# Optimization experiments

Measured on AMD Instinct MI355X. Metric: run time of the kernel, lower is better.

Reference implementation:

```python
import jax, jax.numpy as jnp
import numpy as np

K_GRID = 20          # grid side -> n1 = 400 nodes, n2 = 760 edges
CONTEXT = 512
HIDDEN = 2 * CONTEXT # per module: hidden_dim = 2*context_size
BATCH = 4096
RHO = 1.0            # ADMM penalty
N_ITERS = 50         # fixed ADMM iterations (differentiable unroll)


def _grid_incidence(k):
    """Node-arc incidence of a k x k grid DAG (right + down edges)."""
    n = k * k
    edges = []
    for i in range(k):
        for j in range(k):
            u = i * k + j
            if j + 1 < k:
                edges.append((u, i * k + j + 1))
            if i + 1 < k:
                edges.append((u, (i + 1) * k + j))
    m = len(edges)
    A = np.zeros((n, m), np.float32)
    for e, (u, v) in enumerate(edges):
        A[u, e] = 1.0   # outflow
        A[v, e] = -1.0  # inflow
    b = np.zeros(n, np.float32)
    b[0] = 1.0      # source
    b[n - 1] = -1.0 # sink
    return A, b


def setup_inputs() -> dict:
    key = jax.random.key(0)
    k_d, k_w1, k_b1, k_w2, k_b2 = jax.random.split(key, 5)
    A_np, b_np = _grid_incidence(K_GRID)
    n2 = A_np.shape[1]
    d = jax.random.normal(k_d, (BATCH, CONTEXT), dtype=jnp.float32)
    s1 = 1.0 / np.sqrt(CONTEXT)
    s2 = 1.0 / np.sqrt(HIDDEN)
    W1 = jax.random.uniform(k_w1, (HIDDEN, CONTEXT), jnp.float32, -s1, s1)
    b1 = jax.random.uniform(k_b1, (HIDDEN,), jnp.float32, -s1, s1)
    W2 = jax.random.uniform(k_w2, (n2, HIDDEN), jnp.float32, -s2, s2)
    b2 = jax.random.uniform(k_b2, (n2,), jnp.float32, -s2, s2)
    return {"d": d, "W1": W1, "b1": b1, "W2": W2, "b2": b2,
            "A": jnp.asarray(A_np), "b_eq": jnp.asarray(b_np)}


def reference(d, W1, b1, W2, b2, A, b_eq):
    # MLP router: fc_1 -> LeakyReLU(0.1) -> fc_2
    h = d @ W1.T + b1
    h = jnp.where(h >= 0, h, 0.1 * h)
    w = h @ W2.T + b2  # [B, n2] edge costs

    # QP: min_x w^T x + 0.5||x||^2  s.t.  A x = b_eq, x >= 0
    # Batched ADMM with equality-constrained x-update (KKT solve via pinv(AA^T)).
    M = jnp.linalg.pinv(A @ A.T)  # [n1, n1], symmetric
    z = jnp.zeros_like(w)
    u = jnp.zeros_like(w)
    x = jnp.zeros_like(w)

    def step(carry, _):
        x, z, u = carry
        v = RHO * (z - u) - w                       # [B, n2]
        nu = (v @ A.T - (1.0 + RHO) * b_eq) @ M     # [B, n1] dual of Ax=b
        x = (v - nu @ A) / (1.0 + RHO)              # satisfies A x = b
        z = jnp.maximum(x + u, 0.0)                 # projection onto x >= 0
        u = u + x - z
        return (x, z, u), None

    (x, z, u), _ = jax.lax.scan(step, (x, z, u), None, length=N_ITERS)
    return x  # [B, n2], primal solution (matches CvxpyLayer's variable x)
```

## Files before the change

kernel.cpp:

```cpp
#include <hip/hip_runtime.h>

#define KG 20
#define N1 400
#define N2 760
#define BATCH 4096
#define NITER 50
#define PI_F 3.14159265897932f

typedef __attribute__((ext_vector_type(8))) short bf16x8;
typedef __attribute__((ext_vector_type(4))) float f32x4;

#define WSYNC() asm volatile("s_waitcnt lgkmcnt(0)" ::: "memory")

__device__ __forceinline__ float bf2f(unsigned short u) {
    unsigned int x = ((unsigned int)u) << 16;
    union { unsigned int i; float f; } c; c.i = x; return c.f;
}
__device__ __forceinline__ unsigned short f2bf(float f) {
    union { float f; unsigned int i; } c; c.f = f;
    unsigned int r = c.i + 0x7FFFu + ((c.i >> 16) & 1u);
    return (unsigned short)(r >> 16);
}

constexpr double CPI = 3.14159265358979323846;
constexpr double ccos(double x) {
    constexpr double TP = 6.28318530717958647692;
    long long k = (long long)(x / TP);
    double r = x - (double)k * TP;
    if (r > CPI)  r -= TP;
    if (r < -CPI) r += TP;
    double r2 = r * r, term = 1.0, s = 1.0;
    for (int n = 1; n <= 15; ++n) { term *= -r2 / ((2.0 * n - 1.0) * (2.0 * n)); s += term; }
    return s;
}
struct Tbl { float phi[20][20]; float lam[20]; };
constexpr Tbl mk_tbl() {
    Tbl t{};
    for (int i = 0; i < 20; ++i)
        for (int a = 0; a < 20; ++a) {
            double na = (a == 0) ? 0.22360679774997896964 : 0.31622776601683793320;
            t.phi[i][a] = (float)(na * ccos(CPI * (double)a * ((double)i + 0.5) / 20.0));
        }
    for (int a = 0; a < 20; ++a) t.lam[a] = (float)(2.0 - 2.0 * ccos(CPI * (double)a / 20.0));
    return t;
}
static constexpr Tbl TB = mk_tbl();

__global__ void detect_dtype(const float* beq_as_f32, int* flag) {
    if (threadIdx.x == 0) {
        float v = beq_as_f32[0];
        *flag = (v > 0.5f && v < 1.5f) ? 0 : 1;
    }
}

__global__ void conv_biases(const void* b1, const void* b2, float* b1f, float* b2f,
                            const int* flag) {
    int i = blockIdx.x * 256 + threadIdx.x;
    int f = *flag;
    if (i < 1024)
        b1f[i] = f ? bf2f(((const unsigned short*)b1)[i]) : ((const float*)b1)[i];
    else if (i < 1024 + 760) {
        int j = i - 1024;
        b2f[j] = f ? bf2f(((const unsigned short*)b2)[j]) : ((const float*)b2)[j];
    }
}

template<bool LEAKY>
__global__ __launch_bounds__(256) void gemm_bt_bf16(
        const void* __restrict__ A,
        const void* __restrict__ B,
        const float* __restrict__ bias,
        unsigned short* __restrict__ C,
        int M, int N, int K, const int* __restrict__ flagp, int aUseFlag) {
    __shared__ unsigned short As[128 * 34];
    __shared__ unsigned short Bs[64 * 34];
    const int f   = *flagp;
    const int aBf = aUseFlag ? f : 1;
    const int bBf = f;
    const int tid  = threadIdx.x;
    const int m0   = blockIdx.x * 128;
    const int n0   = blockIdx.y * 64;
    const int wave = tid >> 6, lane = tid & 63;
    const int wm   = (wave & 1) * 64, wn = (wave >> 1) * 32;
    const int fr   = lane & 15;
    const int kc   = (lane >> 4) * 8;

    const int ra = tid >> 1, ca = (tid & 1) * 16;
    const int rb = tid >> 2, cb = (tid & 3) * 8;
    const int rbg = (n0 + rb < N) ? (n0 + rb) : (N - 1);

    f32x4 acc[4][2];
#pragma unroll
    for (int a = 0; a < 4; a++)
#pragma unroll
        for (int b = 0; b < 2; b++) acc[a][b] = (f32x4){0.f, 0.f, 0.f, 0.f};

    for (int k0 = 0; k0 < K; k0 += 32) {
        size_t aoff = (size_t)(m0 + ra) * K + k0 + ca;
        uint4 av0, av1;
        if (aBf) {
            av0 = *(const uint4*)&((const unsigned short*)A)[aoff];
            av1 = *(const uint4*)&((const unsigned short*)A)[aoff + 8];
        } else {
            const float* Af = (const float*)A;
            float4 f0 = *(const float4*)&Af[aoff];
            float4 f1 = *(const float4*)&Af[aoff + 4];
            float4 f2 = *(const float4*)&Af[aoff + 8];
            float4 f3 = *(const float4*)&Af[aoff + 12];
            av0.x = ((unsigned)f2bf(f0.y) << 16) | f2bf(f0.x);
            av0.y = ((unsigned)f2bf(f0.w) << 16) | f2bf(f0.z);
            av0.z = ((unsigned)f2bf(f1.y) << 16) | f2bf(f1.x);
            av0.w = ((unsigned)f2bf(f1.w) << 16) | f2bf(f1.z);
            av1.x = ((unsigned)f2bf(f2.y) << 16) | f2bf(f2.x);
            av1.y = ((unsigned)f2bf(f2.w) << 16) | f2bf(f2.z);
            av1.z = ((unsigned)f2bf(f3.y) << 16) | f2bf(f3.x);
            av1.w = ((unsigned)f2bf(f3.w) << 16) | f2bf(f3.z);
        }
        size_t boff = (size_t)rbg * K + k0 + cb;
        uint4 bv;
        if (bBf) bv = *(const uint4*)&((const unsigned short*)B)[boff];
        else {
            const float* Bf = (const float*)B;
            float4 f0 = *(const float4*)&Bf[boff];
            float4 f1 = *(const float4*)&Bf[boff + 4];
            bv.x = ((unsigned)f2bf(f0.y) << 16) | f2bf(f0.x);
            bv.y = ((unsigned)f2bf(f0.w) << 16) | f2bf(f0.z);
            bv.z = ((unsigned)f2bf(f1.y) << 16) | f2bf(f1.x);
            bv.w = ((unsigned)f2bf(f1.w) << 16) | f2bf(f1.z);
        }
        *(uint4*)&As[ra * 34 + ca]     = av0;
        *(uint4*)&As[ra * 34 + ca + 8] = av1;
        *(uint4*)&Bs[rb * 34 + cb]     = bv;
        __syncthreads();

        bf16x8 af[4], bfm[2];
#pragma unroll
        for (int a = 0; a < 4; a++) af[a]  = *(const bf16x8*)&As[(wm + a * 16 + fr) * 34 + kc];
#pragma unroll
        for (int b = 0; b < 2; b++) bfm[b] = *(const bf16x8*)&Bs[(wn + b * 16 + fr) * 34 + kc];
#pragma unroll
        for (int a = 0; a < 4; a++)
#pragma unroll
            for (int b = 0; b < 2; b++)
                acc[a][b] = __builtin_amdgcn_mfma_f32_16x16x32_bf16(af[a], bfm[b], acc[a][b], 0, 0, 0);
        __syncthreads();
    }
#pragma unroll
    for (int a = 0; a < 4; a++)
#pragma unroll
        for (int b = 0; b < 2; b++) {
            int col = n0 + wn + b * 16 + (lane & 15);
            if (col < N) {
                float bs = bias[col];
#pragma unroll
                for (int r = 0; r < 4; r++) {
                    int row = m0 + wm + a * 16 + (lane >> 4) * 4 + r;
                    float v = acc[a][b][r] + bs;
                    if (LEAKY) v = v >= 0.f ? v : 0.1f * v;
                    C[(size_t)row * N + col] = f2bf(v);
                }
            }
        }
}

#define SREG 448
__global__ __launch_bounds__(256, 2) void admm_kernel(
        const unsigned short* __restrict__ wglob,
        void* __restrict__ out, const int* __restrict__ flagp) {
    __shared__ float buf[8 * SREG];

    const int tid  = threadIdx.x;
    const int wid  = tid >> 6;
    const int lane = tid & 63;
    const int q    = lane >> 5;
    const int li   = lane & 31;
    const int sample = blockIdx.x * 8 + wid * 2 + q;
    const int flag = *flagp;

    if (li < 20) {
        const int i = li;
        float* B = &buf[(wid * 2 + q) * SREG];
        const size_t gb = (size_t)sample * N2;

        float wh[20], wv[20];
        if (i < 19) {
#pragma unroll
            for (int j = 0; j < 19; ++j) {
                wh[j] = bf2f(wglob[gb + 39 * i + 2 * j]);
                wv[j] = bf2f(wglob[gb + 39 * i + 2 * j + 1]);
            }
            wh[19] = 0.f;
            wv[19] = bf2f(wglob[gb + 39 * i + 38]);
        } else {
#pragma unroll
            for (int j = 0; j < 19; ++j) { wh[j] = bf2f(wglob[gb + 741 + j]); wv[j] = 0.f; }
            wh[19] = 0.f; wv[19] = 0.f;
        }

        float g[20];
        {
            float lamB = 2.f - 2.f * cosf(PI_F * (float)li / 20.f);
#pragma unroll
            for (int a = 0; a < 20; ++a) g[a] = 1.f / (TB.lam[a] + lamB);
            if (li == 0) g[0] = 0.f;
        }

        float sh[20], sv[20];
#pragma unroll
        for (int j = 0; j < 20; ++j) { sh[j] = 0.f; sv[j] = 0.f; }

        const int rup = (i > 0)  ? i - 1 : 0;
        const int rdn = (i < 19) ? i + 1 : i;

#pragma unroll 1
        for (int it = 0; it < NITER; ++it) {
            float vh[20], vv[20];
#pragma unroll
            for (int j = 0; j < 20; ++j) {
                vh[j] = fabsf(sh[j]) - wh[j];
                vv[j] = fabsf(sv[j]) - wv[j];
            }
#pragma unroll
            for (int j = 0; j < 20; j += 4)
                *(f32x4*)&B[20 * i + j] = (f32x4){vv[j], vv[j + 1], vv[j + 2], vv[j + 3]};
            WSYNC();
            float vvUp[20];
#pragma unroll
            for (int j = 0; j < 20; j += 4) {
                f32x4 t = *(f32x4*)&B[20 * rup + j];
                vvUp[j] = t[0]; vvUp[j + 1] = t[1]; vvUp[j + 2] = t[2]; vvUp[j + 3] = t[3];
            }
            WSYNC();
            float r[20];
#pragma unroll
            for (int j = 0; j < 20; ++j) {
                float acc = ((j < 19) ? vh[j] : 0.f) + vv[j];
                if (j > 0) acc -= vh[j - 1];
                acc -= (i > 0) ? vvUp[j] : 0.f;
                r[j] = acc;
            }
            r[0]  -= (i == 0)  ? 2.f : 0.f;
            r[19] += (i == 19) ? 2.f : 0.f;

            float e[10], o[10];
#pragma unroll
            for (int jj = 0; jj < 10; ++jj) { e[jj] = r[jj] + r[19 - jj]; o[jj] = r[jj] - r[19 - jj]; }
#pragma unroll
            for (int b = 0; b < 20; ++b) {
                float a;
                if ((b & 1) == 0) {
                    a = e[0] * TB.phi[0][b];
#pragma unroll
                    for (int jj = 1; jj < 10; ++jj) a += e[jj] * TB.phi[jj][b];
                } else {
                    a = o[0] * TB.phi[0][b];
#pragma unroll
                    for (int jj = 1; jj < 10; ++jj) a += o[jj] * TB.phi[jj][b];
                }
                B[22 * b + i] = a;
            }
            WSYNC();
            float t2[20];
#pragma unroll
            for (int k = 0; k < 20; k += 2) {
                float2 p = *(const float2*)&B[22 * li + k];
                t2[k] = p.x; t2[k + 1] = p.y;
            }
            WSYNC();
            float e2[10], o2[10];
#pragma unroll
            for (int kk = 0; kk < 10; ++kk) { e2[kk] = t2[kk] + t2[19 - kk]; o2[kk] = t2[kk] - t2[19 - kk]; }
            float v2[20];
#pragma unroll
            for (int a = 0; a < 20; ++a) {
                float acc;
                if ((a & 1) == 0) {
                    acc = e2[0] * TB.phi[0][a];
#pragma unroll
                    for (int kk = 1; kk < 10; ++kk) acc += e2[kk] * TB.phi[kk][a];
                } else {
                    acc = o2[0] * TB.phi[0][a];
#pragma unroll
                    for (int kk = 1; kk < 10; ++kk) acc += o2[kk] * TB.phi[kk][a];
                }
                v2[a] = acc * g[a];
            }
#pragma unroll
            for (int ii = 0; ii < 10; ++ii) {
                float E = v2[0] * TB.phi[ii][0];
#pragma unroll
                for (int m = 1; m < 10; ++m) E += v2[2 * m] * TB.phi[ii][2 * m];
                float O = v2[1] * TB.phi[ii][1];
#pragma unroll
                for (int m = 1; m < 10; ++m) O += v2[2 * m + 1] * TB.phi[ii][2 * m + 1];
                B[22 * ii + i]        = E + O;
                B[22 * (19 - ii) + i] = E - O;
            }
            WSYNC();
            float t3[20];
#pragma unroll
            for (int b = 0; b < 20; b += 2) {
                float2 p = *(const float2*)&B[22 * li + b];
                t3[b] = p.x; t3[b + 1] = p.y;
            }
            WSYNC();
            float nu[20];
#pragma unroll
            for (int jj = 0; jj < 10; ++jj) {
                float E = t3[0] * TB.phi[jj][0];
#pragma unroll
                for (int m = 1; m < 10; ++m) E += t3[2 * m] * TB.phi[jj][2 * m];
                float O = t3[1] * TB.phi[jj][1];
#pragma unroll
                for (int m = 1; m < 10; ++m) O += t3[2 * m + 1] * TB.phi[jj][2 * m + 1];
                nu[jj]      = E + O;
                nu[19 - jj] = E - O;
            }
#pragma unroll
            for (int j = 0; j < 20; j += 4)
                *(f32x4*)&B[20 * i + j] = (f32x4){nu[j], nu[j + 1], nu[j + 2], nu[j + 3]};
            WSYNC();
            float nuDn[20];
#pragma unroll
            for (int j = 0; j < 20; j += 4) {
                f32x4 t = *(f32x4*)&B[20 * rdn + j];
                nuDn[j] = t[0]; nuDn[j + 1] = t[1]; nuDn[j + 2] = t[2]; nuDn[j + 3] = t[3];
            }
            WSYNC();
#pragma unroll
            for (int j = 0; j < 20; ++j) {
                float xv = 0.5f * (vv[j] - nu[j] + nuDn[j]);
                sv[j] = xv + fminf(sv[j], 0.f);
                float xh = 0.f;
                if (j < 19) {
                    xh = 0.5f * (vh[j] - nu[j] + nu[j + 1]);
                    sh[j] = xh + fminf(sh[j], 0.f);
                }
                if (it == NITER - 1) {
                    if (i < 19) {
                        if (j < 19) {
                            if (flag) {
                                ((unsigned short*)out)[gb + 39 * i + 2 * j]     = f2bf(xh);
                                ((unsigned short*)out)[gb + 39 * i + 2 * j + 1] = f2bf(xv);
                            } else {
                                ((float*)out)[gb + 39 * i + 2 * j]     = xh;
                                ((float*)out)[gb + 39 * i + 2 * j + 1] = xv;
                            }
                        } else {
                            if (flag) ((unsigned short*)out)[gb + 39 * i + 38] = f2bf(xv);
                            else      ((float*)out)[gb + 39 * i + 38] = xv;
                        }
                    } else if (j < 19) {
                        if (flag) ((unsigned short*)out)[gb + 741 + j] = f2bf(xh);
                        else      ((float*)out)[gb + 741 + j] = xh;
                    }
                }
            }
        }
    }
}

extern "C" void kernel_launch(void* const* d_in, const int* in_sizes, int n_in,
                              void* d_out, int out_size, void* d_ws, size_t ws_size,
                              hipStream_t stream) {
    (void)in_sizes; (void)n_in; (void)out_size; (void)ws_size;
    const void* d   = d_in[0];
    const void* W1  = d_in[1];
    const void* b1  = d_in[2];
    const void* W2  = d_in[3];
    const void* b2  = d_in[4];
    const void* beq = d_in[6];

    char* ws = (char*)d_ws;
    int*            flag  = (int*)ws;
    float*          b1_f  = (float*)(ws + 256);
    float*          b2_f  = (float*)(ws + 4608);
    unsigned short* h_bf  = (unsigned short*)(ws + 8192);
    unsigned short* w_bf  = (unsigned short*)(ws + 8396800);

    detect_dtype<<<1, 64, 0, stream>>>((const float*)beq, flag);
    conv_biases<<<7, 256, 0, stream>>>(b1, b2, b1_f, b2_f, flag);

    gemm_bt_bf16<true ><<<dim3(32, 16), 256, 0, stream>>>(d,    W1, b1_f, h_bf, 4096, 1024, 512,  flag, 1);
    gemm_bt_bf16<false><<<dim3(32, 12), 256, 0, stream>>>(h_bf, W2, b2_f, w_bf, 4096, 760,  1024, flag, 0);

    admm_kernel<<<BATCH / 8, 256, 0, stream>>>(w_bf, d_out, flag);
}
```

Before: 349.4 us.

## Inline dtype detection, register-prefetch GEMM tiles, and hand-code DCT MACs with immediates

Drops the separate dtype-detection and bias-conversion kernels: each kernel now reads b_eq directly to infer dtype and converts the bias inline, which removes two launches. The GEMM loads the next k-tile into registers before computing on the current tile in shared memory, overlapping global loads with MFMA work. The DCT transforms in the ADMM loop are rewritten as inline-asm v_mul/v_fmac chains with literal constant operands so table coefficients never occupy registers. The inline asm may block compiler scheduling, and the halved table relies on the even/odd symmetry of the basis.

```diff
diff --git a/kernel.cpp b/kernel.cpp
--- a/kernel.cpp
+++ b/kernel.cpp
@@ -5,7 +5,7 @@
 #define N2 760
 #define BATCH 4096
 #define NITER 50
-#define PI_F 3.14159265897932f
+#define PI_F 3.14159265358979f
 
 typedef __attribute__((ext_vector_type(8))) short bf16x8;
 typedef __attribute__((ext_vector_type(4))) float f32x4;
@@ -33,10 +33,10 @@
     for (int n = 1; n <= 15; ++n) { term *= -r2 / ((2.0 * n - 1.0) * (2.0 * n)); s += term; }
     return s;
 }
-struct Tbl { float phi[20][20]; float lam[20]; };
+struct Tbl { float phi[10][20]; float lam[20]; };
 constexpr Tbl mk_tbl() {
     Tbl t{};
-    for (int i = 0; i < 20; ++i)
+    for (int i = 0; i < 10; ++i)
         for (int a = 0; a < 20; ++a) {
             double na = (a == 0) ? 0.22360679774997896964 : 0.31622776601683793320;
             t.phi[i][a] = (float)(na * ccos(CPI * (double)a * ((double)i + 0.5) / 20.0));
@@ -46,35 +46,44 @@
 }
 static constexpr Tbl TB = mk_tbl();
 
-__global__ void detect_dtype(const float* beq_as_f32, int* flag) {
-    if (threadIdx.x == 0) {
-        float v = beq_as_f32[0];
-        *flag = (v > 0.5f && v < 1.5f) ? 0 : 1;
-    }
-}
-
-__global__ void conv_biases(const void* b1, const void* b2, float* b1f, float* b2f,
-                            const int* flag) {
-    int i = blockIdx.x * 256 + threadIdx.x;
-    int f = *flag;
-    if (i < 1024)
-        b1f[i] = f ? bf2f(((const unsigned short*)b1)[i]) : ((const float*)b1)[i];
-    else if (i < 1024 + 760) {
-        int j = i - 1024;
-        b2f[j] = f ? bf2f(((const unsigned short*)b2)[j]) : ((const float*)b2)[j];
-    }
+#define CBITS(c) ((int)__builtin_bit_cast(unsigned int, (float)(c)))
+#define VMUL(d, c, s) asm("v_mul_f32 %0, %1, %2"  : "=v"(d) : "i"(CBITS(c)), "v"(s))
+#define VMAC(d, c, s) asm("v_fmac_f32 %0, %1, %2" : "+v"(d) : "i"(CBITS(c)), "v"(s))
+
+#define MACC10(acc, a, B) do { \
+    VMUL(acc, TB.phi[0][B], a[0]); VMAC(acc, TB.phi[1][B], a[1]); \
+    VMAC(acc, TB.phi[2][B], a[2]); VMAC(acc, TB.phi[3][B], a[3]); \
+    VMAC(acc, TB.phi[4][B], a[4]); VMAC(acc, TB.phi[5][B], a[5]); \
+    VMAC(acc, TB.phi[6][B], a[6]); VMAC(acc, TB.phi[7][B], a[7]); \
+    VMAC(acc, TB.phi[8][B], a[8]); VMAC(acc, TB.phi[9][B], a[9]); } while (0)
+#define MACE10(acc, a, II) do { \
+    VMUL(acc, TB.phi[II][0],  a[0]);  VMAC(acc, TB.phi[II][2],  a[2]); \
+    VMAC(acc, TB.phi[II][4],  a[4]);  VMAC(acc, TB.phi[II][6],  a[6]); \
+    VMAC(acc, TB.phi[II][8],  a[8]);  VMAC(acc, TB.phi[II][10], a[10]); \
+    VMAC(acc, TB.phi[II][12], a[12]); VMAC(acc, TB.phi[II][14], a[14]); \
+    VMAC(acc, TB.phi[II][16], a[16]); VMAC(acc, TB.phi[II][18], a[18]); } while (0)
+#define MACO10(acc, a, II) do { \
+    VMUL(acc, TB.phi[II][1],  a[1]);  VMAC(acc, TB.phi[II][3],  a[3]); \
+    VMAC(acc, TB.phi[II][5],  a[5]);  VMAC(acc, TB.phi[II][7],  a[7]); \
+    VMAC(acc, TB.phi[II][9],  a[9]);  VMAC(acc, TB.phi[II][11], a[11]); \
+    VMAC(acc, TB.phi[II][13], a[13]); VMAC(acc, TB.phi[II][15], a[15]); \
+    VMAC(acc, TB.phi[II][17], a[17]); VMAC(acc, TB.phi[II][19], a[19]); } while (0)
+
+__device__ __forceinline__ int detect_flag(const float* beqf) {
+    float v = beqf[0];
+    return (v > 0.5f && v < 1.5f) ? 0 : 1;
 }
 
 template<bool LEAKY>
 __global__ __launch_bounds__(256) void gemm_bt_bf16(
         const void* __restrict__ A,
         const void* __restrict__ B,
-        const float* __restrict__ bias,
+        const void* __restrict__ biasRaw,
         unsigned short* __restrict__ C,
-        int M, int N, int K, const int* __restrict__ flagp, int aUseFlag) {
+        int M, int N, int K, const float* __restrict__ beqf, int aUseFlag) {
     __shared__ unsigned short As[128 * 34];
     __shared__ unsigned short Bs[64 * 34];
-    const int f   = *flagp;
+    const int f   = detect_flag(beqf);
     const int aBf = aUseFlag ? f : 1;
     const int bBf = f;
     const int tid  = threadIdx.x;
@@ -89,15 +98,9 @@
     const int rb = tid >> 2, cb = (tid & 3) * 8;
     const int rbg = (n0 + rb < N) ? (n0 + rb) : (N - 1);
 
-    f32x4 acc[4][2];
-#pragma unroll
-    for (int a = 0; a < 4; a++)
-#pragma unroll
-        for (int b = 0; b < 2; b++) acc[a][b] = (f32x4){0.f, 0.f, 0.f, 0.f};
-
-    for (int k0 = 0; k0 < K; k0 += 32) {
+    uint4 av0, av1, bv;
+    auto load_tiles = [&](int k0) {
         size_t aoff = (size_t)(m0 + ra) * K + k0 + ca;
-        uint4 av0, av1;
         if (aBf) {
             av0 = *(const uint4*)&((const unsigned short*)A)[aoff];
             av1 = *(const uint4*)&((const unsigned short*)A)[aoff + 8];
@@ -117,7 +120,6 @@
             av1.w = ((unsigned)f2bf(f3.w) << 16) | f2bf(f3.z);
         }
         size_t boff = (size_t)rbg * K + k0 + cb;
-        uint4 bv;
         if (bBf) bv = *(const uint4*)&((const unsigned short*)B)[boff];
         else {
             const float* Bf = (const float*)B;
@@ -128,11 +130,24 @@
             bv.z = ((unsigned)f2bf(f1.y) << 16) | f2bf(f1.x);
             bv.w = ((unsigned)f2bf(f1.w) << 16) | f2bf(f1.z);
         }
+    };
+
+    f32x4 acc[4][2];
+#pragma unroll
+    for (int a = 0; a < 4; a++)
+#pragma unroll
+        for (int b = 0; b < 2; b++) acc[a][b] = (f32x4){0.f, 0.f, 0.f, 0.f};
+
+    load_tiles(0);
+    for (int k0 = 0; k0 < K; k0 += 32) {
         *(uint4*)&As[ra * 34 + ca]     = av0;
         *(uint4*)&As[ra * 34 + ca + 8] = av1;
         *(uint4*)&Bs[rb * 34 + cb]     = bv;
         __syncthreads();
 
+        int kn = (k0 + 32 < K) ? (k0 + 32) : k0;
+        load_tiles(kn);
+
         bf16x8 af[4], bfm[2];
 #pragma unroll
         for (int a = 0; a < 4; a++) af[a]  = *(const bf16x8*)&As[(wm + a * 16 + fr) * 34 + kc];
@@ -151,7 +166,8 @@
         for (int b = 0; b < 2; b++) {
             int col = n0 + wn + b * 16 + (lane & 15);
             if (col < N) {
-                float bs = bias[col];
+                float bs = f ? bf2f(((const unsigned short*)biasRaw)[col])
+                             : ((const float*)biasRaw)[col];
 #pragma unroll
                 for (int r = 0; r < 4; r++) {
                     int row = m0 + wm + a * 16 + (lane >> 4) * 4 + r;
@@ -166,7 +182,7 @@
 #define SREG 448
 __global__ __launch_bounds__(256, 2) void admm_kernel(
         const unsigned short* __restrict__ wglob,
-        void* __restrict__ out, const int* __restrict__ flagp) {
+        void* __restrict__ out, const float* __restrict__ beqf) {
     __shared__ float buf[8 * SREG];
 
     const int tid  = threadIdx.x;
@@ -175,7 +191,7 @@
     const int q    = lane >> 5;
     const int li   = lane & 31;
     const int sample = blockIdx.x * 8 + wid * 2 + q;
-    const int flag = *flagp;
+    const int flag = detect_flag(beqf);
 
     if (li < 20) {
         const int i = li;
@@ -245,20 +261,19 @@
             float e[10], o[10];
 #pragma unroll
             for (int jj = 0; jj < 10; ++jj) { e[jj] = r[jj] + r[19 - jj]; o[jj] = r[jj] - r[19 - jj]; }
-#pragma unroll
-            for (int b = 0; b < 20; ++b) {
-                float a;
-                if ((b & 1) == 0) {
-                    a = e[0] * TB.phi[0][b];
-#pragma unroll
-                    for (int jj = 1; jj < 10; ++jj) a += e[jj] * TB.phi[jj][b];
-                } else {
-                    a = o[0] * TB.phi[0][b];
-#pragma unroll
-                    for (int jj = 1; jj < 10; ++jj) a += o[jj] * TB.phi[jj][b];
-                }
-                B[22 * b + i] = a;
-            }
+            float t1[20];
+            MACC10(t1[0],  e, 0);  MACC10(t1[1],  o, 1);
+            MACC10(t1[2],  e, 2);  MACC10(t1[3],  o, 3);
+            MACC10(t1[4],  e, 4);  MACC10(t1[5],  o, 5);
+            MACC10(t1[6],  e, 6);  MACC10(t1[7],  o, 7);
+            MACC10(t1[8],  e, 8);  MACC10(t1[9],  o, 9);
+            MACC10(t1[10], e, 10); MACC10(t1[11], o, 11);
+            MACC10(t1[12], e, 12); MACC10(t1[13], o, 13);
+            MACC10(t1[14], e, 14); MACC10(t1[15], o, 15);
+            MACC10(t1[16], e, 16); MACC10(t1[17], o, 17);
+            MACC10(t1[18], e, 18); MACC10(t1[19], o, 19);
+#pragma unroll
+            for (int b = 0; b < 20; ++b) B[22 * b + i] = t1[b];
             WSYNC();
             float t2[20];
 #pragma unroll
@@ -270,32 +285,25 @@
             float e2[10], o2[10];
 #pragma unroll
             for (int kk = 0; kk < 10; ++kk) { e2[kk] = t2[kk] + t2[19 - kk]; o2[kk] = t2[kk] - t2[19 - kk]; }
+            float u[20];
+            MACC10(u[0],  e2, 0);  MACC10(u[1],  o2, 1);
+            MACC10(u[2],  e2, 2);  MACC10(u[3],  o2, 3);
+            MACC10(u[4],  e2, 4);  MACC10(u[5],  o2, 5);
+            MACC10(u[6],  e2, 6);  MACC10(u[7],  o2, 7);
+            MACC10(u[8],  e2, 8);  MACC10(u[9],  o2, 9);
+            MACC10(u[10], e2, 10); MACC10(u[11], o2, 11);
+            MACC10(u[12], e2, 12); MACC10(u[13], o2, 13);
+            MACC10(u[14], e2, 14); MACC10(u[15], o2, 15);
+            MACC10(u[16], e2, 16); MACC10(u[17], o2, 17);
+            MACC10(u[18], e2, 18); MACC10(u[19], o2, 19);
             float v2[20];
 #pragma unroll
-            for (int a = 0; a < 20; ++a) {
-                float acc;
-                if ((a & 1) == 0) {
-                    acc = e2[0] * TB.phi[0][a];
-#pragma unroll
-                    for (int kk = 1; kk < 10; ++kk) acc += e2[kk] * TB.phi[kk][a];
-                } else {
-                    acc = o2[0] * TB.phi[0][a];
-#pragma unroll
-                    for (int kk = 1; kk < 10; ++kk) acc += o2[kk] * TB.phi[kk][a];
-                }
-                v2[a] = acc * g[a];
-            }
-#pragma unroll
-            for (int ii = 0; ii < 10; ++ii) {
-                float E = v2[0] * TB.phi[ii][0];
-#pragma unroll
-                for (int m = 1; m < 10; ++m) E += v2[2 * m] * TB.phi[ii][2 * m];
-                float O = v2[1] * TB.phi[ii][1];
-#pragma unroll
-                for (int m = 1; m < 10; ++m) O += v2[2 * m + 1] * TB.phi[ii][2 * m + 1];
-                B[22 * ii + i]        = E + O;
-                B[22 * (19 - ii) + i] = E - O;
-            }
+            for (int a = 0; a < 20; ++a) v2[a] = u[a] * g[a];
+#define YROW(II) { float E, O; MACE10(E, v2, II); MACO10(O, v2, II); \
+                   B[22 * II + i] = E + O; B[22 * (19 - II) + i] = E - O; }
+            YROW(0) YROW(1) YROW(2) YROW(3) YROW(4)
+            YROW(5) YROW(6) YROW(7) YROW(8) YROW(9)
+#undef YROW
             WSYNC();
             float t3[20];
 #pragma unroll
@@ -305,17 +313,11 @@
             }
             WSYNC();
             float nu[20];
-#pragma unroll
-            for (int jj = 0; jj < 10; ++jj) {
-                float E = t3[0] * TB.phi[jj][0];
-#pragma unroll
-                for (int m = 1; m < 10; ++m) E += t3[2 * m] * TB.phi[jj][2 * m];
-                float O = t3[1] * TB.phi[jj][1];
-#pragma unroll
-                for (int m = 1; m < 10; ++m) O += t3[2 * m + 1] * TB.phi[jj][2 * m + 1];
-                nu[jj]      = E + O;
-                nu[19 - jj] = E - O;
-            }
+#define NUROW(JJ) { float E, O; MACE10(E, t3, JJ); MACO10(O, t3, JJ); \
+                    nu[JJ] = E + O; nu[19 - JJ] = E - O; }
+            NUROW(0) NUROW(1) NUROW(2) NUROW(3) NUROW(4)
+            NUROW(5) NUROW(6) NUROW(7) NUROW(8) NUROW(9)
+#undef NUROW
 #pragma unroll
             for (int j = 0; j < 20; j += 4)
                 *(f32x4*)&B[20 * i + j] = (f32x4){nu[j], nu[j + 1], nu[j + 2], nu[j + 3]};
@@ -364,25 +366,19 @@
                               void* d_out, int out_size, void* d_ws, size_t ws_size,
                               hipStream_t stream) {
     (void)in_sizes; (void)n_in; (void)out_size; (void)ws_size;
-    const void* d   = d_in[0];
-    const void* W1  = d_in[1];
-    const void* b1  = d_in[2];
-    const void* W2  = d_in[3];
-    const void* b2  = d_in[4];
-    const void* beq = d_in[6];
+    const void*  d   = d_in[0];
+    const void*  W1  = d_in[1];
+    const void*  b1  = d_in[2];
+    const void*  W2  = d_in[3];
+    const void*  b2  = d_in[4];
+    const float* beq = (const float*)d_in[6];
 
     char* ws = (char*)d_ws;
-    int*            flag  = (int*)ws;
-    float*          b1_f  = (float*)(ws + 256);
-    float*          b2_f  = (float*)(ws + 4608);
-    unsigned short* h_bf  = (unsigned short*)(ws + 8192);
-    unsigned short* w_bf  = (unsigned short*)(ws + 8396800);
-
-    detect_dtype<<<1, 64, 0, stream>>>((const float*)beq, flag);
-    conv_biases<<<7, 256, 0, stream>>>(b1, b2, b1_f, b2_f, flag);
-
-    gemm_bt_bf16<true ><<<dim3(32, 16), 256, 0, stream>>>(d,    W1, b1_f, h_bf, 4096, 1024, 512,  flag, 1);
-    gemm_bt_bf16<false><<<dim3(32, 12), 256, 0, stream>>>(h_bf, W2, b2_f, w_bf, 4096, 760,  1024, flag, 0);
-
-    admm_kernel<<<BATCH / 8, 256, 0, stream>>>(w_bf, d_out, flag);
-}
+    unsigned short* h_bf = (unsigned short*)(ws);
+    unsigned short* w_bf = (unsigned short*)(ws + 8388608);
+
+    gemm_bt_bf16<true ><<<dim3(32, 16), 256, 0, stream>>>(d,    W1, b1, h_bf, 4096, 1024, 512,  beq, 1);
+    gemm_bt_bf16<false><<<dim3(32, 12), 256, 0, stream>>>(h_bf, W2, b2, w_bf, 4096, 760,  1024, beq, 0);
+
+    admm_kernel<<<BATCH / 8, 256, 0, stream>>>(w_bf, d_out, beq);
+}
```

Result: slower. 360.2 us (+3.1%).
